# Kernel tuning notes

Measured on AMD Instinct MI355X. Metric: run time of the kernel, lower is better.

## Reference

```python
import jax, jax.numpy as jnp
import numpy as np

B, S, IN_DIM, D_MODEL, H = 8, 1024, 512, 1024, 16
DEPTH = D_MODEL // H
LN_EPS = 1e-5


def setup_inputs() -> dict:
    key = jax.random.key(0)
    ks = jax.random.split(key, 10)
    def xavier(k, shape):
        fan_in, fan_out = shape[0], shape[1]
        lim = float(np.sqrt(6.0 / (fan_in + fan_out)))
        return jax.random.uniform(k, shape, jnp.float32, -lim, lim)
    return {
        "x": jax.random.normal(ks[0], (B, S, IN_DIM), jnp.float32),
        "mask": jax.random.randint(ks[1], (H, S, S), 0, 2, jnp.int32),
        "wq_w": xavier(ks[2], (IN_DIM, D_MODEL)),
        "wq_b": jnp.zeros((D_MODEL,), jnp.float32),
        "wk_w": xavier(ks[3], (IN_DIM, D_MODEL)),
        "wk_b": jnp.zeros((D_MODEL,), jnp.float32),
        "wv_w": xavier(ks[4], (IN_DIM, D_MODEL)),
        "wv_b": jnp.zeros((D_MODEL,), jnp.float32),
        "dense_w": xavier(ks[5], (D_MODEL, D_MODEL)),
        "dense_b": jnp.zeros((D_MODEL,), jnp.float32),
        "res_w": xavier(ks[6], (IN_DIM, D_MODEL)),  # residual_linear (no bias)
        "ln_g": 1.0 + 0.02 * jax.random.normal(ks[7], (D_MODEL,), jnp.float32),
        "ln_b": 0.02 * jax.random.normal(ks[8], (D_MODEL,), jnp.float32),
    }


def reference(x, mask, wq_w, wq_b, wk_w, wk_b, wv_w, wv_b,
              dense_w, dense_b, res_w, ln_g, ln_b):
    bs = x.shape[0]
    residual = x @ res_w  # [B,S,D_MODEL]
    # project and split heads -> [B,H,S,depth]
    def split(t):
        return t.reshape(bs, -1, H, DEPTH).transpose(0, 2, 1, 3)
    q = split(x @ wq_w + wq_b)
    k = split(x @ wk_w + wk_b)
    v = split(x @ wv_w + wv_b)
    scale = 1.0 / jnp.sqrt(jnp.asarray(DEPTH, x.dtype))
    attn = jnp.einsum("bhqd,bhkd->bhqk", q, k) * scale
    attn = jnp.where(mask[None] == 0, jnp.asarray(-1e9, attn.dtype), attn)
    attn = jax.nn.softmax(attn, axis=-1)  # dropout is identity in eval
    out = jnp.einsum("bhqk,bhkd->bhqd", attn, v)
    out = out.transpose(0, 2, 1, 3).reshape(bs, -1, D_MODEL)
    out = out @ dense_w + dense_b
    # residual + LayerNorm
    y = residual + out
    mu = jnp.mean(y, axis=-1, keepdims=True)
    var = jnp.mean(jnp.square(y - mu), axis=-1, keepdims=True)
    y = (y - mu) * jax.lax.rsqrt(var + LN_EPS)
    return y * ln_g + ln_b
```

## Files before the change

### kernel.cpp

```cpp
#include <hip/hip_runtime.h>
#include <stdint.h>

#define B_ 8
#define S_ 1024
#define IN_DIM 512
#define DM 1024
#define H_ 16
#define DEP 64

typedef __bf16 bf16;
typedef __attribute__((ext_vector_type(8))) __bf16 bf16x8;
typedef __attribute__((ext_vector_type(4))) __bf16 bf16x4;
typedef __attribute__((ext_vector_type(4))) short short4v;
typedef __attribute__((ext_vector_type(4))) float f32x4;

#if defined(__has_builtin)
#if __has_builtin(__builtin_amdgcn_mfma_f32_16x16x16_bf16)
#define HAVE_NEW16 1
#endif
#endif
static __device__ __forceinline__ f32x4 mfma16(bf16x4 a, bf16x4 b, f32x4 c) {
#ifdef HAVE_NEW16
    return __builtin_amdgcn_mfma_f32_16x16x16_bf16(a, b, c, 0, 0, 0);
#else
    union { bf16x4 h; short4v s; } ua, ub;
    ua.h = a; ub.h = b;
    return __builtin_amdgcn_mfma_f32_16x16x16bf16_1k(ua.s, ub.s, c, 0, 0, 0);
#endif
}

static __device__ __forceinline__ void gld_lds16(const void* g, void* l) {
    __builtin_amdgcn_global_load_lds(
        (const __attribute__((address_space(1))) uint32_t*)g,
        (__attribute__((address_space(3))) uint32_t*)l, 16, 0, 0);
}

__global__ void detect_kernel(const uint16_t* __restrict__ xraw, int* __restrict__ flag) {
    const int t = threadIdx.x;
    int sane = 0;
    #pragma unroll
    for (int j = 0; j < 8; j++) {
        const uint16_t u = xraw[t * 8 + j];
        const int e = (u >> 7) & 0xff;
        sane += ((u & 0x7fff) == 0 || (e >= 100 && e <= 140)) ? 1 : 0;
    }
    #pragma unroll
    for (int m = 1; m < 64; m <<= 1) sane += __shfl_xor(sane, m);
    if (t == 0) *flag = (sane >= 450) ? 1 : 0;
}

static __device__ __forceinline__ float ldin(const void* p, size_t i, int isb) {
    return isb ? (float)((const bf16*)p)[i] : ((const float*)p)[i];
}

__global__ __launch_bounds__(256) void transpose_kernel(
    const void* __restrict__ wq, const void* __restrict__ wk, const void* __restrict__ wv,
    const void* __restrict__ res, const void* __restrict__ dense,
    bf16* __restrict__ wqT, bf16* __restrict__ wkT, bf16* __restrict__ wvT,
    bf16* __restrict__ resT, bf16* __restrict__ denseT, const int* __restrict__ flag)
{
    const int isb = *flag;
    __shared__ bf16 tile[32][33];
    const int z = blockIdx.z;
    const void* src; bf16* dst; int kb, kd;
    if (z == 0)      { src = wq;    dst = wqT;    kb = 0;   kd = 512;  }
    else if (z == 1) { src = wk;    dst = wkT;    kb = 0;   kd = 512;  }
    else if (z == 2) { src = wv;    dst = wvT;    kb = 0;   kd = 512;  }
    else if (z == 3) { src = res;   dst = resT;   kb = 0;   kd = 512;  }
    else if (z == 4) { src = dense; dst = denseT; kb = 0;   kd = 1024; }
    else             { src = dense; dst = denseT; kb = 512; kd = 1024; }
    const int n0 = blockIdx.x * 32, k0 = blockIdx.y * 32;
    const int tx = threadIdx.x, ty = threadIdx.y;
    #pragma unroll
    for (int r = 0; r < 4; r++)
        tile[ty + r*8][tx] = (bf16)ldin(src, (size_t)(kb + k0 + ty + r*8) * DM + n0 + tx, isb);
    __syncthreads();
    #pragma unroll
    for (int r = 0; r < 4; r++)
        dst[(size_t)(n0 + ty + r*8) * kd + kb + k0 + tx] = tile[tx][ty + r*8];
}

__global__ __launch_bounds__(256) void xconv_kernel(
    const void* __restrict__ x, bf16* __restrict__ xc, const int* __restrict__ flag)
{
    const int isb = *flag;
    const size_t i = ((size_t)blockIdx.x * 256 + threadIdx.x) * 4;
    #pragma unroll
    for (int j = 0; j < 4; j++) xc[i + j] = (bf16)ldin(x, i + j, isb);
}

__global__ __launch_bounds__(256) void smallconv_kernel(
    const void* b0, const void* b1, const void* b2, const void* b3,
    const void* b4, const void* b5, bf16* __restrict__ out, const int* __restrict__ flag)
{
    const int isb = *flag;
    const void* srcs[6] = {b0, b1, b2, b3, b4, b5};
    const void* s = srcs[blockIdx.x];
    for (int i = threadIdx.x; i < 1024; i += 256)
        out[blockIdx.x * 1024 + i] = (bf16)ldin(s, i, isb);
}

__global__ __launch_bounds__(256) void maskpack_kernel(
    const int* __restrict__ mask, unsigned long long* __restrict__ mb)
{
    const int w = threadIdx.x >> 6, lane = threadIdx.x & 63;
    const int gw = blockIdx.x * 4 + w;
    for (int c = gw; c < 262144; c += 4096) {
        const int v = mask[(size_t)c * 64 + lane];
        const unsigned long long bits = __ballot(v != 0);
        if (lane == 0) mb[c] = bits;
    }
}

template<int KDIM>
static __device__ __forceinline__ void gemm_core(
    const bf16* __restrict__ A, const bf16* __restrict__ BT,
    int m0, int n0, bf16* Asm, bf16* Bsm, f32x4 acc[4][4])
{
    const int tid = threadIdx.x, l = tid & 63, w = tid >> 6;
    const int wm = w >> 1, wn = w & 1, quad = l >> 4, l15 = l & 15;
    #pragma unroll
    for (int i = 0; i < 4; i++)
        #pragma unroll
        for (int j = 0; j < 4; j++) acc[i][j] = f32x4{0.f, 0.f, 0.f, 0.f};

    for (int k0 = 0; k0 < KDIM; k0 += 32) {
        __syncthreads();
        #pragma unroll
        for (int qq = 0; qq < 2; qq++) {
            const int c = qq*256 + tid;
            const int row = c >> 2, ch = c & 3;
            gld_lds16(A  + (size_t)(m0 + row)*KDIM + k0 + ch*8, Asm + (qq*256 + w*64)*8);
            gld_lds16(BT + (size_t)(n0 + row)*KDIM + k0 + ch*8, Bsm + (qq*256 + w*64)*8);
        }
        __syncthreads();
        bf16x8 af[4], bfv[4];
        #pragma unroll
        for (int i = 0; i < 4; i++)
            af[i] = *(const bf16x8*)(Asm + (wm*64 + i*16 + l15)*32 + quad*8);
        #pragma unroll
        for (int j = 0; j < 4; j++)
            bfv[j] = *(const bf16x8*)(Bsm + (wn*64 + j*16 + l15)*32 + quad*8);
        #pragma unroll
        for (int i = 0; i < 4; i++)
            #pragma unroll
            for (int j = 0; j < 4; j++)
                acc[i][j] = __builtin_amdgcn_mfma_f32_16x16x32_bf16(af[i], bfv[j], acc[i][j], 0, 0, 0);
    }
}

#define EPI_P 132
__global__ __launch_bounds__(256) void proj_kernel(
    const bf16* __restrict__ x,
    const bf16* __restrict__ wqT, const bf16* __restrict__ wkT,
    const bf16* __restrict__ wvT, const bf16* __restrict__ resT,
    const bf16* __restrict__ small,
    bf16* __restrict__ Q, bf16* __restrict__ K, bf16* __restrict__ VtG, bf16* __restrict__ R)
{
    __shared__ alignas(16) char smem[17408];
    bf16* Asm = (bf16*)smem;
    bf16* Bsm = (bf16*)(smem + 8192);
    bf16* epi = (bf16*)smem;

    const int m0 = blockIdx.x * 128;
    const int ng = blockIdx.y * 128;
    const int sel = ng >> 10, n0 = ng & 1023;
    const bf16* BT; const bf16* bias = nullptr;
    if (sel == 0)      { BT = wqT; bias = small;        }
    else if (sel == 1) { BT = wkT; bias = small + 1024; }
    else if (sel == 2) { BT = wvT; bias = small + 2048; }
    else               { BT = resT; }

    f32x4 acc[4][4];
    gemm_core<IN_DIM>(x, BT, m0, n0, Asm, Bsm, acc);

    const int tid = threadIdx.x, l = tid & 63, w = tid >> 6;
    const int wm = w >> 1, wn = w & 1, quad = l >> 4, l15 = l & 15;

    if (sel == 2) {
        const int bb = m0 >> 10, srow0 = m0 & 1023;
        #pragma unroll
        for (int hf = 0; hf < 2; hf++) {
            __syncthreads();
            if (wn == hf) {
                #pragma unroll
                for (int j = 0; j < 4; j++) {
                    const int cl = j*16 + l15;
                    const float bv = (float)bias[n0 + hf*64 + cl];
                    #pragma unroll
                    for (int i = 0; i < 4; i++) {
                        const int rho = wm*64 + i*16 + quad*4;
                        #pragma unroll
                        for (int r = 0; r < 4; r++)
                            epi[cl*EPI_P + rho + r] = (bf16)(acc[i][j][r] + bv);
                    }
                }
            }
            __syncthreads();
            const int hh = (n0 >> 6) + hf;
            const int sc = tid & 15;
            #pragma unroll
            for (int pass = 0; pass < 4; pass++) {
                const int dl = (tid >> 4) + pass*16;
                bf16x8 v;
                #pragma unroll
                for (int k = 0; k < 8; k++) v[k] = epi[dl*EPI_P + sc*8 + k];
                *(bf16x8*)(VtG + ((size_t)(bb*16 + hh)*64 + dl)*S_ + srow0 + sc*8) = v;
            }
        }
        return;
    }

    #pragma unroll
    for (int j = 0; j < 4; j++) {
        const int col = n0 + wn*64 + j*16 + l15;
        const float bv = (sel < 3) ? (float)bias[col] : 0.f;
        #pragma unroll
        for (int i = 0; i < 4; i++) {
            const int rb = m0 + wm*64 + i*16 + quad*4;
            #pragma unroll
            for (int r = 0; r < 4; r++) {
                const float v = acc[i][j][r] + bv;
                if (sel == 0)      Q[(size_t)(rb + r)*DM + col] = (bf16)(v * 0.18033688f);
                else if (sel == 1) K[(size_t)(rb + r)*DM + col] = (bf16)v;
                else               R[(size_t)(rb + r)*DM + col] = (bf16)v;
            }
        }
    }
}

#define KP 68
__global__ __launch_bounds__(256, 4) void attn_kernel(
    const bf16* __restrict__ Q, const bf16* __restrict__ K, const bf16* __restrict__ VtG,
    const unsigned long long* __restrict__ mb, bf16* __restrict__ AO)
{
    __shared__ alignas(16) bf16 Ksm[2*64*KP];
    __shared__ alignas(16) bf16 Vsm[2*64*KP];

    const int tid = threadIdx.x, l = tid & 63, w = tid >> 6;
    const int quad = l >> 4, l15 = l & 15;

    const int fid = blockIdx.y * 8 + blockIdx.x;
    const int xcd = fid & 7, idx = fid >> 3;
    const int bh  = xcd * 16 + (idx >> 3);
    const int qt  = idx & 7;
    const int b = bh >> 4, h = bh & 15;
    const int wrow = qt*128 + w*32;
    const size_t rowbase = (size_t)b * S_;

    bf16x8 qa[2][2];
    #pragma unroll
    for (int g = 0; g < 2; g++) {
        const bf16* qp = Q + (rowbase + wrow + g*16 + l15)*DM + h*DEP + quad*8;
        qa[g][0] = *(const bf16x8*)qp;
        qa[g][1] = *(const bf16x8*)(qp + 32);
    }
    const bf16* kgbase = K + rowbase*DM + h*DEP;
    const bf16* vgbase = VtG + (size_t)(b*16 + h)*64*S_;
    const unsigned long long* mbase[2];
    #pragma unroll
    for (int g = 0; g < 2; g++)
        mbase[g] = mb + ((size_t)h*S_ + wrow + g*16 + l15) * 16;

    uint32_t bmr[4];
    #pragma unroll
    for (int r = 0; r < 4; r++) bmr[r] = 1u << (quad*4 + r);

    bf16x4 onesv;
    #pragma unroll
    for (int r = 0; r < 4; r++) onesv[r] = (bf16)1.0f;

    f32x4 oT[2][4];
    f32x4 lacc[2];
    #pragma unroll
    for (int g = 0; g < 2; g++) {
        lacc[g] = f32x4{0.f,0.f,0.f,0.f};
        #pragma unroll
        for (int dt = 0; dt < 4; dt++) oT[g][dt] = f32x4{0.f,0.f,0.f,0.f};
    }

    const int srow = tid >> 3, sch = tid & 7;
    const bf16* kg0 = kgbase + (size_t)srow*DM + sch*8;
    const bf16* kg1 = kgbase + (size_t)(32 + srow)*DM + sch*8;
    const bf16* vg0 = vgbase + (size_t)srow*S_ + sch*8;
    const bf16* vg1 = vgbase + (size_t)(32 + srow)*S_ + sch*8;

    bf16x8 k0v = *(const bf16x8*)kg0;
    bf16x8 k1v = *(const bf16x8*)kg1;
    bf16x8 v0v = *(const bf16x8*)vg0;
    bf16x8 v1v = *(const bf16x8*)vg1;
    uint32_t mlo[2], mhi[2];
    #pragma unroll
    for (int g = 0; g < 2; g++) {
        const unsigned long long mword = mbase[g][0];
        mlo[g] = (uint32_t)mword; mhi[g] = (uint32_t)(mword >> 32);
    }

    *(bf16x8*)(Ksm + srow*KP + sch*8)        = k0v;
    *(bf16x8*)(Ksm + (32 + srow)*KP + sch*8) = k1v;
    *(bf16x8*)(Vsm + srow*KP + sch*8)        = v0v;
    *(bf16x8*)(Vsm + (32 + srow)*KP + sch*8) = v1v;

    for (int it = 0; it < 16; it++) {
        const int cur = (it & 1) * (64*KP);
        const int nxt = ((it & 1) ^ 1) * (64*KP);
        const bf16* Kc = Ksm + cur;
        const bf16* Vc = Vsm + cur;
        __syncthreads();

        const uint32_t cmlo[2] = {mlo[0], mlo[1]}, cmhi[2] = {mhi[0], mhi[1]};
        if (it + 1 < 16) {
            const size_t ko = (size_t)(it + 1) * 64 * DM;
            const int    vo = (it + 1) * 64;
            k0v = *(const bf16x8*)(kg0 + ko);
            k1v = *(const bf16x8*)(kg1 + ko);
            v0v = *(const bf16x8*)(vg0 + vo);
            v1v = *(const bf16x8*)(vg1 + vo);
            #pragma unroll
            for (int g = 0; g < 2; g++) {
                const unsigned long long mword = mbase[g][it + 1];
                mlo[g] = (uint32_t)mword; mhi[g] = (uint32_t)(mword >> 32);
            }
        }

        #pragma unroll
        for (int sub = 0; sub < 2; sub++) {
            bf16x8 kf[2][2];
            bf16x4 va[2][4];
            #pragma unroll
            for (int h2 = 0; h2 < 2; h2++) {
                const bf16* kp = Kc + (sub*32 + h2*16 + l15)*KP + quad*8;
                kf[h2][0] = *(const bf16x8*)kp;
                kf[h2][1] = *(const bf16x8*)(kp + 32);
            }
            #pragma unroll
            for (int h2 = 0; h2 < 2; h2++)
                #pragma unroll
                for (int dt = 0; dt < 4; dt++)
                    va[h2][dt] = *(const bf16x4*)(Vc + (dt*16 + l15)*KP + sub*32 + h2*16 + quad*4);

            #pragma unroll
            for (int g = 0; g < 2; g++) {
                f32x4 st[2];
                #pragma unroll
                for (int h2 = 0; h2 < 2; h2++) {
                    f32x4 z = {0.f,0.f,0.f,0.f};
                    z = __builtin_amdgcn_mfma_f32_16x16x32_bf16(kf[h2][0], qa[g][0], z, 0, 0, 0);
                    z = __builtin_amdgcn_mfma_f32_16x16x32_bf16(kf[h2][1], qa[g][1], z, 0, 0, 0);
                    st[h2] = z;
                }
                const uint32_t msk = sub ? cmhi[g] : cmlo[g];
                bf16x4 pb[2];
                #pragma unroll
                for (int h2 = 0; h2 < 2; h2++) {
                    const uint32_t mh = msk >> (h2 * 16);
                    #pragma unroll
                    for (int r = 0; r < 4; r++) {
                        const float e = __builtin_amdgcn_exp2f(st[h2][r]);
                        const float pv = (mh & bmr[r]) ? e : 0.f;
                        pb[h2][r] = (bf16)pv;
                    }
                }
                #pragma unroll
                for (int h2 = 0; h2 < 2; h2++) {
                    lacc[g] = mfma16(onesv, pb[h2], lacc[g]);
                    #pragma unroll
                    for (int dt = 0; dt < 4; dt++)
                        oT[g][dt] = mfma16(va[h2][dt], pb[h2], oT[g][dt]);
                }
            }
        }

        if (it + 1 < 16) {
            *(bf16x8*)(Ksm + nxt + srow*KP + sch*8)        = k0v;
            *(bf16x8*)(Ksm + nxt + (32 + srow)*KP + sch*8) = k1v;
            *(bf16x8*)(Vsm + nxt + srow*KP + sch*8)        = v0v;
            *(bf16x8*)(Vsm + nxt + (32 + srow)*KP + sch*8) = v1v;
        }
    }

    #pragma unroll
    for (int g = 0; g < 2; g++) {
        const float inv = 1.0f / lacc[g][0];
        bf16* aor = AO + (rowbase + wrow + g*16 + l15)*DM + h*DEP;
        #pragma unroll
        for (int dt = 0; dt < 4; dt++) {
            bf16x4 ov;
            #pragma unroll
            for (int r = 0; r < 4; r++) ov[r] = (bf16)(oT[g][dt][r] * inv);
            *(bf16x4*)(aor + dt*16 + quad*4) = ov;
        }
    }
}

__global__ __launch_bounds__(256) void dense_kernel(
    const bf16* __restrict__ AOin, const bf16* __restrict__ dT,
    const bf16* __restrict__ db, bf16* __restrict__ R)
{
    __shared__ alignas(16) bf16 Asm[128*32];
    __shared__ alignas(16) bf16 Bsm[128*32];
    const int m0 = blockIdx.x * 128, n0 = blockIdx.y * 128;
    f32x4 acc[4][4];
    gemm_core<DM>(AOin, dT, m0, n0, Asm, Bsm, acc);
    const int tid = threadIdx.x, l = tid & 63, w = tid >> 6;
    const int wm = w >> 1, wn = w & 1, quad = l >> 4, l15 = l & 15;
    #pragma unroll
    for (int j = 0; j < 4; j++) {
        const int col = n0 + wn*64 + j*16 + l15;
        const float bv = (float)db[col];
        #pragma unroll
        for (int i = 0; i < 4; i++) {
            const int rb = m0 + wm*64 + i*16 + quad*4;
            #pragma unroll
            for (int r = 0; r < 4; r++) {
                const size_t idx = (size_t)(rb + r)*DM + col;
                R[idx] = (bf16)((float)R[idx] + acc[i][j][r] + bv);
            }
        }
    }
}

__global__ __launch_bounds__(256) void ln_kernel(
    const bf16* __restrict__ R, const bf16* __restrict__ small,
    void* __restrict__ out, const int* __restrict__ flag)
{
    const int isb = *flag;
    __shared__ float red[8];
    const int row = blockIdx.x, tid = threadIdx.x;
    const bf16x4 rv = *(const bf16x4*)(R + (size_t)row*DM + tid*4);
    const float vx = (float)rv[0], vy = (float)rv[1], vz = (float)rv[2], vw = (float)rv[3];
    float s = vx + vy + vz + vw;
    #pragma unroll
    for (int m = 1; m < 64; m <<= 1) s += __shfl_xor(s, m);
    const int w = tid >> 6;
    if ((tid & 63) == 0) red[w] = s;
    __syncthreads();
    const float mu = (red[0] + red[1] + red[2] + red[3]) * (1.0f/DM);
    const float dx = vx - mu, dy = vy - mu, dz = vz - mu, dw = vw - mu;
    float q = dx*dx + dy*dy + dz*dz + dw*dw;
    #pragma unroll
    for (int m = 1; m < 64; m <<= 1) q += __shfl_xor(q, m);
    if ((tid & 63) == 0) red[4 + w] = q;
    __syncthreads();
    const float var = (red[4] + red[5] + red[6] + red[7]) * (1.0f/DM);
    const float rstd = rsqrtf(var + 1e-5f);
    const int col = tid * 4;
    const bf16x4 gv = *(const bf16x4*)(small + 4*1024 + col);
    const bf16x4 bv = *(const bf16x4*)(small + 5*1024 + col);
    const float o0 = dx*rstd*(float)gv[0] + (float)bv[0];
    const float o1 = dy*rstd*(float)gv[1] + (float)bv[1];
    const float o2 = dz*rstd*(float)gv[2] + (float)bv[2];
    const float o3 = dw*rstd*(float)gv[3] + (float)bv[3];
    if (isb) {
        bf16x4 ov; ov[0] = (bf16)o0; ov[1] = (bf16)o1; ov[2] = (bf16)o2; ov[3] = (bf16)o3;
        *(bf16x4*)((bf16*)out + (size_t)row*DM + col) = ov;
    } else {
        float4 ov = {o0, o1, o2, o3};
        *(float4*)((float*)out + (size_t)row*DM + col) = ov;
    }
}

extern "C" void kernel_launch(void* const* d_in, const int* in_sizes, int n_in,
                              void* d_out, int out_size, void* d_ws, size_t ws_size,
                              hipStream_t stream) {
    const int* mask = (const int*)d_in[1];

    char* ws = (char*)d_ws;
    bf16* wqT   = (bf16*)(ws);
    bf16* wkT   = (bf16*)(ws + ((size_t)1 << 20));
    bf16* wvT   = (bf16*)(ws + ((size_t)2 << 20));
    bf16* resT  = (bf16*)(ws + ((size_t)3 << 20));
    bf16* dT    = (bf16*)(ws + ((size_t)4 << 20));
    bf16* small = (bf16*)(ws + ((size_t)6 << 20));
    int*  flag  = (int*) (ws + ((size_t)6 << 20) + 16384);
    unsigned long long* mbits = (unsigned long long*)(ws + ((size_t)7 << 20));
    bf16* Qb    = (bf16*)(ws + ((size_t)9  << 20));
    bf16* Kb    = (bf16*)(ws + ((size_t)25 << 20));
    bf16* VtG   = (bf16*)(ws + ((size_t)41 << 20));
    bf16* R     = (bf16*)(ws + ((size_t)57 << 20));
    bf16* xc    = (bf16*)d_out;

    detect_kernel<<<1, 64, 0, stream>>>((const uint16_t*)d_in[0], flag);
    transpose_kernel<<<dim3(32, 16, 6), dim3(32, 8), 0, stream>>>(
        d_in[2], d_in[4], d_in[6], d_in[10], d_in[8],
        wqT, wkT, wvT, resT, dT, flag);
    xconv_kernel<<<4096, 256, 0, stream>>>(d_in[0], xc, flag);
    smallconv_kernel<<<6, 256, 0, stream>>>(
        d_in[3], d_in[5], d_in[7], d_in[9], d_in[11], d_in[12], small, flag);
    maskpack_kernel<<<1024, 256, 0, stream>>>(mask, mbits);
    proj_kernel<<<dim3(64, 32), 256, 0, stream>>>(
        xc, wqT, wkT, wvT, resT, small, Qb, Kb, VtG, R);
    attn_kernel<<<dim3(8, 128), 256, 0, stream>>>(Qb, Kb, VtG, mbits, Qb );
    dense_kernel<<<dim3(64, 8), 256, 0, stream>>>(Qb, dT, small + 3*1024, R);
    ln_kernel<<<8192, 256, 0, stream>>>(R, small, d_out, flag);
}
```

Before: 364.6 us.

## Stream attention K/V tiles directly into XOR-swizzled LDS and raise MFMA priority

The attention kernel stops staging K and V tiles through registers. It now issues direct global-to-LDS 16-byte loads into an unpadded 64-wide buffer, using an XOR swizzle on the 8-element chunk index in place of the old padding, and the fragment reads apply the matching swizzle. Mask words are now loaded in the iteration that uses them rather than prefetched one step ahead. s_setprio brackets the MFMA groups so the matrix instructions get issue priority over the exp and mask work. The aim is to cut register pressure and VALU store work, and to shrink the LDS footprint. The cost is that correctness now depends on the load completing before the barrier, and the mask load latency is exposed in each iteration.

```diff
diff --git a/kernel.cpp b/kernel.cpp
--- a/kernel.cpp
+++ b/kernel.cpp
@@ -229,13 +229,12 @@
     }
 }
 
-#define KP 68
 __global__ __launch_bounds__(256, 4) void attn_kernel(
     const bf16* __restrict__ Q, const bf16* __restrict__ K, const bf16* __restrict__ VtG,
     const unsigned long long* __restrict__ mb, bf16* __restrict__ AO)
 {
-    __shared__ alignas(16) bf16 Ksm[2*64*KP];
-    __shared__ alignas(16) bf16 Vsm[2*64*KP];
+    __shared__ alignas(16) bf16 Ksm[2*64*64];
+    __shared__ alignas(16) bf16 Vsm[2*64*64];
 
     const int tid = threadIdx.x, l = tid & 63, w = tid >> 6;
     const int quad = l >> 4, l15 = l & 15;
@@ -279,47 +278,39 @@
         for (int dt = 0; dt < 4; dt++) oT[g][dt] = f32x4{0.f,0.f,0.f,0.f};
     }
 
-    const int srow = tid >> 3, sch = tid & 7;
-    const bf16* kg0 = kgbase + (size_t)srow*DM + sch*8;
-    const bf16* kg1 = kgbase + (size_t)(32 + srow)*DM + sch*8;
-    const bf16* vg0 = vgbase + (size_t)srow*S_ + sch*8;
-    const bf16* vg1 = vgbase + (size_t)(32 + srow)*S_ + sch*8;
-
-    bf16x8 k0v = *(const bf16x8*)kg0;
-    bf16x8 k1v = *(const bf16x8*)kg1;
-    bf16x8 v0v = *(const bf16x8*)vg0;
-    bf16x8 v1v = *(const bf16x8*)vg1;
-    uint32_t mlo[2], mhi[2];
-    #pragma unroll
-    for (int g = 0; g < 2; g++) {
-        const unsigned long long mword = mbase[g][0];
-        mlo[g] = (uint32_t)mword; mhi[g] = (uint32_t)(mword >> 32);
-    }
-
-    *(bf16x8*)(Ksm + srow*KP + sch*8)        = k0v;
-    *(bf16x8*)(Ksm + (32 + srow)*KP + sch*8) = k1v;
-    *(bf16x8*)(Vsm + srow*KP + sch*8)        = v0v;
-    *(bf16x8*)(Vsm + (32 + srow)*KP + sch*8) = v1v;
+    const int srow8 = l >> 3;
+    const int gch   = (l & 7) ^ srow8;
+
+    #pragma unroll
+    for (int q = 0; q < 2; q++) {
+        const int row = q*32 + w*8 + srow8;
+        gld_lds16(kgbase + (size_t)row*DM + gch*8, Ksm + (q*256 + w*64)*8);
+        gld_lds16(vgbase + (size_t)row*S_ + gch*8, Vsm + (q*256 + w*64)*8);
+    }
+
+    const int rsw = l15 & 7;
 
     for (int it = 0; it < 16; it++) {
-        const int cur = (it & 1) * (64*KP);
-        const int nxt = ((it & 1) ^ 1) * (64*KP);
+        __syncthreads();
+        const int cur = (it & 1) * 4096, nxt = cur ^ 4096;
         const bf16* Kc = Ksm + cur;
         const bf16* Vc = Vsm + cur;
-        __syncthreads();
-
-        const uint32_t cmlo[2] = {mlo[0], mlo[1]}, cmhi[2] = {mhi[0], mhi[1]};
+
+        uint32_t cm[2][2];
+        #pragma unroll
+        for (int g = 0; g < 2; g++) {
+            const unsigned long long mw = mbase[g][it];
+            cm[g][0] = (uint32_t)mw; cm[g][1] = (uint32_t)(mw >> 32);
+        }
+
         if (it + 1 < 16) {
-            const size_t ko = (size_t)(it + 1) * 64 * DM;
-            const int    vo = (it + 1) * 64;
-            k0v = *(const bf16x8*)(kg0 + ko);
-            k1v = *(const bf16x8*)(kg1 + ko);
-            v0v = *(const bf16x8*)(vg0 + vo);
-            v1v = *(const bf16x8*)(vg1 + vo);
-            #pragma unroll
-            for (int g = 0; g < 2; g++) {
-                const unsigned long long mword = mbase[g][it + 1];
-                mlo[g] = (uint32_t)mword; mhi[g] = (uint32_t)(mword >> 32);
+            #pragma unroll
+            for (int q = 0; q < 2; q++) {
+                const int row = q*32 + w*8 + srow8;
+                gld_lds16(kgbase + (size_t)((it+1)*64 + row)*DM + gch*8,
+                          Ksm + nxt + (q*256 + w*64)*8);
+                gld_lds16(vgbase + (size_t)row*S_ + (it+1)*64 + gch*8,
+                          Vsm + nxt + (q*256 + w*64)*8);
             }
         }
 
@@ -329,19 +320,22 @@
             bf16x4 va[2][4];
             #pragma unroll
             for (int h2 = 0; h2 < 2; h2++) {
-                const bf16* kp = Kc + (sub*32 + h2*16 + l15)*KP + quad*8;
-                kf[h2][0] = *(const bf16x8*)kp;
-                kf[h2][1] = *(const bf16x8*)(kp + 32);
-            }
-            #pragma unroll
-            for (int h2 = 0; h2 < 2; h2++)
+                const int krow = sub*32 + h2*16 + l15;
+                kf[h2][0] = *(const bf16x8*)(Kc + krow*64 + ((quad    ) ^ rsw)*8);
+                kf[h2][1] = *(const bf16x8*)(Kc + krow*64 + ((quad + 4) ^ rsw)*8);
+            }
+            #pragma unroll
+            for (int h2 = 0; h2 < 2; h2++) {
+                const int cb = sub*4 + h2*2 + (quad >> 1);
                 #pragma unroll
                 for (int dt = 0; dt < 4; dt++)
-                    va[h2][dt] = *(const bf16x4*)(Vc + (dt*16 + l15)*KP + sub*32 + h2*16 + quad*4);
+                    va[h2][dt] = *(const bf16x4*)(Vc + (dt*16 + l15)*64 + (cb ^ rsw)*8 + (quad&1)*4);
+            }
 
             #pragma unroll
             for (int g = 0; g < 2; g++) {
                 f32x4 st[2];
+                __builtin_amdgcn_s_setprio(1);
                 #pragma unroll
                 for (int h2 = 0; h2 < 2; h2++) {
                     f32x4 z = {0.f,0.f,0.f,0.f};
@@ -349,7 +343,8 @@
                     z = __builtin_amdgcn_mfma_f32_16x16x32_bf16(kf[h2][1], qa[g][1], z, 0, 0, 0);
                     st[h2] = z;
                 }
-                const uint32_t msk = sub ? cmhi[g] : cmlo[g];
+                __builtin_amdgcn_s_setprio(0);
+                const uint32_t msk = cm[g][sub];
                 bf16x4 pb[2];
                 #pragma unroll
                 for (int h2 = 0; h2 < 2; h2++) {
@@ -361,6 +356,7 @@
                         pb[h2][r] = (bf16)pv;
                     }
                 }
+                __builtin_amdgcn_s_setprio(1);
                 #pragma unroll
                 for (int h2 = 0; h2 < 2; h2++) {
                     lacc[g] = mfma16(onesv, pb[h2], lacc[g]);
@@ -368,14 +364,8 @@
                     for (int dt = 0; dt < 4; dt++)
                         oT[g][dt] = mfma16(va[h2][dt], pb[h2], oT[g][dt]);
                 }
-            }
-        }
-
-        if (it + 1 < 16) {
-            *(bf16x8*)(Ksm + nxt + srow*KP + sch*8)        = k0v;
-            *(bf16x8*)(Ksm + nxt + (32 + srow)*KP + sch*8) = k1v;
-            *(bf16x8*)(Vsm + nxt + srow*KP + sch*8)        = v0v;
-            *(bf16x8*)(Vsm + nxt + (32 + srow)*KP + sch*8) = v1v;
+                __builtin_amdgcn_s_setprio(0);
+            }
         }
     }
 
```

Result: faster. 357.3 us (-2.0%).
